# Performance work log

Measured on AMD Instinct MI355X. Metric: run time of the kernel, lower is better.

Reference implementation:

```python
import jax, jax.numpy as jnp
import numpy as np

S, B, D, F, E, K = 1024, 2, 512, 2048, 8, 2


def setup_inputs() -> dict:
    key = jax.random.key(0)
    ks = jax.random.split(key, 12)
    s = lambda *sh: 1.0 / np.sqrt(sh[0])
    inp = {
        "x": jax.random.normal(ks[0], (S, B, D), dtype=jnp.float32),
        # gate: nn.Linear(d_model, n_experts)
        "Wg": jax.random.normal(ks[1], (D, E), dtype=jnp.float32) * s(D),
        "bg": jnp.zeros((E,), dtype=jnp.float32),
        # routed experts: stacked FFN params (E copies of expert)
        "W1": jax.random.normal(ks[2], (E, D, F), dtype=jnp.float32) * s(D),
        "b1": jnp.zeros((E, F), dtype=jnp.float32),
        "W2": jax.random.normal(ks[3], (E, F, D), dtype=jnp.float32) * s(F),
        "b2": jnp.zeros((E, D), dtype=jnp.float32),
        # shared expert (single FFN)
        "Ws1": jax.random.normal(ks[4], (D, F), dtype=jnp.float32) * s(D),
        "bs1": jnp.zeros((F,), dtype=jnp.float32),
        "Ws2": jax.random.normal(ks[5], (F, D), dtype=jnp.float32) * s(F),
        "bs2": jnp.zeros((D,), dtype=jnp.float32),
    }
    return inp


def reference(x, Wg, bg, W1, b1, W2, b2, Ws1, bs1, Ws2, bs2):
    # gate_logits: (S, B, E)
    gate_logits = jnp.einsum("sbd,de->sbe", x, Wg) + bg
    # top-k per token (eval mode: k = n_experts_per_token, t = 1.0)
    weights, selected = jax.lax.top_k(gate_logits, K)  # (S,B,K)
    weights = jax.nn.softmax(weights.astype(jnp.float32), axis=-1)
    # combine weights per expert: (S,B,E)
    onehot = jax.nn.one_hot(selected, E, dtype=weights.dtype)  # (S,B,K,E)
    comb = jnp.einsum("sbk,sbke->sbe", weights, onehot)
    # routed experts computed densely, combined with per-token routing weight
    h = jax.nn.relu(jnp.einsum("sbd,edf->sbef", x, W1) + b1)  # (S,B,E,F)
    y = jnp.einsum("sbef,efd->sbed", h, W2) + b2              # (S,B,E,D)
    out = jnp.einsum("sbe,sbed->sbd", comb, y)
    # shared expert, scaled by 1/k
    hs = jax.nn.relu(jnp.einsum("sbd,df->sbf", x, Ws1) + bs1)
    shared = jnp.einsum("sbf,fd->sbd", hs, Ws2) + bs2
    out = out + (1.0 / K) * shared
    return out
```

## Files before the change

### kernel.cpp

```cpp
#include <hip/hip_runtime.h>
#include <hip/hip_bf16.h>
#include <stdint.h>

#define TT 2048
#define DD 512
#define FF 2048
#define EE 8

typedef unsigned short u16;
typedef __attribute__((ext_vector_type(8))) unsigned short ushort8v;
typedef __attribute__((ext_vector_type(8))) short short8;
typedef __attribute__((ext_vector_type(4))) float float4v;

__device__ __forceinline__ u16 f2bf(float f) {
    unsigned u = __float_as_uint(f);
    u += 0x7FFF + ((u >> 16) & 1);
    return (u16)(u >> 16);
}

__device__ __forceinline__ void gl_lds16(const u16* g, u16* l) {
    __builtin_amdgcn_global_load_lds(
        (const __attribute__((address_space(1))) unsigned int*)g,
        (__attribute__((address_space(3))) unsigned int*)l, 16, 0, 0);
}

#define WS_HB   0ull
#define WS_XG   (WS_HB + 6144ull*2048*2)
#define WS_WT1  (WS_XG + 2048ull*512*2)
#define WS_ME   (WS_WT1 + 9ull*2048*512*2)
#define WS_MW   (WS_ME + 16384)
#define WS_RT   (WS_MW + 16384)
#define WS_WROW (WS_RT + 16384)
#define WS_TROW (WS_WROW + 16384)
#define WS_RTG  (WS_TROW + 16384)
#define WS_WT2  (WS_RTG + 128)
#define WS_NEED (WS_WT2 + 9ull*2048*512*2)

__device__ __forceinline__ void conv_unit(int j, const float* __restrict__ srcE,
                                          const float* __restrict__ srcS,
                                          u16* __restrict__ dst,
                                          int R, int C, int shC, u16* Ls) {
    int mid = j >> 8, t2 = j & 255;
    int tr = t2 >> shC, tc = t2 & ((1 << shC) - 1);
    int r0 = tr * 64, c0 = tc * 64;
    const float* src = (mid < 8) ? srcE + (size_t)mid * R * C : srcS;
    u16* dstm = dst + (size_t)mid * R * C;
    int t = threadIdx.x;
#pragma unroll
    for (int i = 0; i < 4; ++i) {
        int rr = (t >> 4) + i * 16;
        int cc = (t & 15) * 4;
        float4v v = *(const float4v*)(src + (size_t)(r0 + rr) * C + c0 + cc);
#pragma unroll
        for (int jx = 0; jx < 4; ++jx) Ls[(cc + jx) * 72 + rr] = f2bf(v[jx]);
    }
    __syncthreads();
#pragma unroll
    for (int jj = 0; jj < 2; ++jj) {
        int slot = t + jj * 256;
        int cc = slot >> 3, r8 = (slot & 7) * 8;
        ushort8v o = *(const ushort8v*)&Ls[cc * 72 + r8];
        *(ushort8v*)(dstm + (size_t)(c0 + cc) * R + r0 + r8) = o;
    }
}

__device__ __forceinline__ void gate_wave(int t, int lane,
                                          const float* __restrict__ x,
                                          const float* __restrict__ Wg,
                                          const float* __restrict__ bg,
                                          int* __restrict__ metaE,
                                          float* __restrict__ metaW,
                                          u16* __restrict__ xg) {
    const float* xp = x + (size_t)t * DD + lane * 8;
    float4v x0 = *(const float4v*)xp;
    float4v x1 = *(const float4v*)(xp + 4);
    float xf[8] = {x0[0], x0[1], x0[2], x0[3], x1[0], x1[1], x1[2], x1[3]};
    float acc[EE] = {0.f, 0.f, 0.f, 0.f, 0.f, 0.f, 0.f, 0.f};
#pragma unroll
    for (int g = 0; g < 8; ++g) {
        const float* wp = Wg + (size_t)(lane * 8 + g) * EE;
        float4v w0 = *(const float4v*)wp;
        float4v w1 = *(const float4v*)(wp + 4);
        acc[0] += xf[g] * w0[0]; acc[1] += xf[g] * w0[1];
        acc[2] += xf[g] * w0[2]; acc[3] += xf[g] * w0[3];
        acc[4] += xf[g] * w1[0]; acc[5] += xf[g] * w1[1];
        acc[6] += xf[g] * w1[2]; acc[7] += xf[g] * w1[3];
    }
#pragma unroll
    for (int off = 1; off < 64; off <<= 1) {
#pragma unroll
        for (int e = 0; e < EE; ++e) acc[e] += __shfl_xor(acc[e], off, 64);
    }
    ushort8v xv;
#pragma unroll
    for (int jx = 0; jx < 4; ++jx) xv[jx] = f2bf(x0[jx]);
#pragma unroll
    for (int jx = 0; jx < 4; ++jx) xv[4 + jx] = f2bf(x1[jx]);
    *(ushort8v*)(xg + (size_t)t * DD + lane * 8) = xv;
    if (lane == 0) {
#pragma unroll
        for (int e = 0; e < EE; ++e) acc[e] += bg[e];
        int e0 = 0; float l0 = acc[0];
#pragma unroll
        for (int e = 1; e < EE; ++e) if (acc[e] > l0) { l0 = acc[e]; e0 = e; }
        int e1 = -1; float l1 = -3.4e38f;
#pragma unroll
        for (int e = 0; e < EE; ++e)
            if (e != e0 && acc[e] > l1) { l1 = acc[e]; e1 = e; }
        float ex = __expf(l1 - l0);
        float w0 = 1.f / (1.f + ex);
        metaE[2 * t] = e0; metaE[2 * t + 1] = e1;
        metaW[2 * t] = w0; metaW[2 * t + 1] = 1.f - w0;
    }
}

__global__ __launch_bounds__(256) void fused1_k(
    const float* __restrict__ x, const float* __restrict__ Wg,
    const float* __restrict__ bg,
    const float* __restrict__ W1, const float* __restrict__ Ws1,
    const float* __restrict__ W2, const float* __restrict__ Ws2,
    float* __restrict__ out, u16* __restrict__ xg,
    u16* __restrict__ Wt1, u16* __restrict__ Wt2,
    int* __restrict__ metaE, float* __restrict__ metaW, int nconv) {
    __shared__ __align__(16) u16 Ls[64 * 72];
    int b = blockIdx.x, tid = threadIdx.x;
    if (b < nconv) {
        if (b < 2304) conv_unit(b, W1, Ws1, Wt1, DD, FF, 5, Ls);
        else          conv_unit(b - 2304, W2, Ws2, Wt2, FF, DD, 3, Ls);
    } else if (b < nconv + 512) {
        int gb = b - nconv;
        gate_wave(gb * 4 + (tid >> 6), tid & 63, x, Wg, bg, metaE, metaW, xg);
    } else {
        int zb = b - nconv - 512;
        float* op = out + (size_t)zb * 8192;
#pragma unroll
        for (int it = 0; it < 8; ++it)
            *(float4v*)(op + it * 1024 + tid * 4) = (float4v){0.f, 0.f, 0.f, 0.f};
    }
}

__global__ __launch_bounds__(256) void conv2_k(const float* __restrict__ W2,
                                               const float* __restrict__ Ws2,
                                               u16* __restrict__ Wt2) {
    __shared__ __align__(16) u16 Ls[64 * 72];
    conv_unit(blockIdx.x, W2, Ws2, Wt2, FF, DD, 3, Ls);
}

__global__ __launch_bounds__(256) void rank_k(const int* __restrict__ metaE,
                                              const float* __restrict__ metaW,
                                              int* __restrict__ routing,
                                              int* __restrict__ rtok,
                                              float* __restrict__ wrow,
                                              int* __restrict__ trow) {
    __shared__ __align__(16) char smem[16384];
    u16* er      = (u16*)smem;
    int* segCnt  = (int*)(smem + 8192);
    int* segBase = (int*)(smem + 10240);
    int* expTot  = (int*)(smem + 12288);
    int tid = threadIdx.x, wv = tid >> 6, lane = tid & 63;
    unsigned long long below = (lane == 0) ? 0ull : ((~0ull) >> (64 - lane));
    for (int s = wv * 16; s < wv * 16 + 16; ++s) {
        int entry = s * 64 + lane;
        int e = metaE[entry];
        int rk = 0;
#pragma unroll
        for (int ee = 0; ee < 8; ++ee) {
            unsigned long long m = __ballot(e == ee);
            if (e == ee) rk = __popcll(m & below);
            if (lane == ee) segCnt[s * 8 + ee] = __popcll(m);
        }
        er[entry] = (u16)(e | (rk << 4));
    }
    __syncthreads();
    if (tid < 8) {
        int s = 0;
        for (int g = 0; g < 64; ++g) { segBase[g * 8 + tid] = s; s += segCnt[g * 8 + tid]; }
        expTot[tid] = s;
    }
    __syncthreads();
    if (tid == 0) {
        int s = 0;
        for (int e = 0; e < 8; ++e) { int c = expTot[e]; expTot[8 + e] = s; s += c; }
    }
    __syncthreads();
    if (tid < 8) { routing[tid] = expTot[8 + tid]; routing[8 + tid] = expTot[tid]; }
    for (int i = 0; i < 16; ++i) {
        int entry = tid + i * 256;
        int v = er[entry];
        int e = v & 15, rk = v >> 4;
        int row = expTot[8 + e] + segBase[(entry >> 6) * 8 + e] + rk;
        rtok[row] = entry >> 1;
        wrow[row] = metaW[entry];
        trow[entry] = row;
    }
}

__global__ __launch_bounds__(256) void gemmA_k(
    const u16* __restrict__ xg, const u16* __restrict__ Wt1,
    const float* __restrict__ b1, const float* __restrict__ bs1,
    const int* __restrict__ routing, const int* __restrict__ rtok,
    u16* __restrict__ hbuf) {
    __shared__ __align__(16) u16 As[2][64 * 64];
    __shared__ __align__(16) u16 Bs[2][128 * 64];
    const int* offs = routing; const int* cnt = routing + 8;
    int j = blockIdx.x, tid = threadIdx.x;
    int rt, ct, Mloc, hRowBase, rowBase; bool routed;
    const u16* Bsrc; const float* bias;
    if (j < 512) {
        rt = j >> 4; ct = j & 15; Mloc = 64; rowBase = rt * 64;
        Bsrc = Wt1 + (size_t)8 * FF * DD; bias = bs1;
        hRowBase = 4096 + rt * 64; routed = false;
    } else {
        int jr = j - 512; int e = jr & 7; int rc = jr >> 3;
        rt = rc >> 4; ct = rc & 15;
        int M = cnt[e]; if (rt * 64 >= M) return;
        Mloc = M - rt * 64; if (Mloc > 64) Mloc = 64;
        rowBase = offs[e] + rt * 64;
        Bsrc = Wt1 + (size_t)e * FF * DD; bias = b1 + e * FF;
        hRowBase = rowBase; routed = true;
    }
    int n0 = ct * 128;
    int lane = tid & 63, w = tid >> 6, ln = lane & 15, quad = lane >> 4;
    int lr8 = lane >> 3;
    int cs = (lane & 7) ^ lr8;
    const u16* ApS[2];
#pragma unroll
    for (int i = 0; i < 2; ++i) {
        int r = w * 16 + i * 8 + lr8;
        int tok;
        if (routed) { int br = rowBase + r; if (br > 4095) br = 4095; tok = rtok[br]; }
        else tok = rowBase + r;
        ApS[i] = xg + (size_t)tok * DD + cs * 8;
    }
    const u16* BpS[4];
#pragma unroll
    for (int i = 0; i < 4; ++i) {
        int r = w * 32 + i * 8 + lr8;
        BpS[i] = Bsrc + (size_t)(n0 + r) * DD + cs * 8;
    }
    float4v acc[2][4];
#pragma unroll
    for (int a = 0; a < 2; ++a)
#pragma unroll
        for (int b = 0; b < 4; ++b) acc[a][b] = (float4v){0.f, 0.f, 0.f, 0.f};

    auto stage = [&](int kt, int pb) {
        u16* Ab = &As[pb][0]; u16* Bb = &Bs[pb][0];
#pragma unroll
        for (int i = 0; i < 2; ++i)
            gl_lds16(ApS[i] + kt * 64, Ab + (w * 16 + i * 8) * 64);
#pragma unroll
        for (int i = 0; i < 4; ++i)
            gl_lds16(BpS[i] + kt * 64, Bb + (w * 32 + i * 8) * 64);
    };

    stage(0, 0);
#pragma unroll
    for (int kt = 0; kt < 8; ++kt) {
        int pb = kt & 1;
        if (kt < 7) {
            stage(kt + 1, pb ^ 1);
            asm volatile("s_waitcnt vmcnt(6)" ::: "memory");
        } else {
            asm volatile("s_waitcnt vmcnt(0)" ::: "memory");
        }
        __builtin_amdgcn_s_barrier();
        __builtin_amdgcn_sched_barrier(0);
        const u16* Ab = &As[pb][0]; const u16* Bb = &Bs[pb][0];
#pragma unroll
        for (int s = 0; s < 2; ++s) {
            int chs = ((s * 4 + quad) ^ (ln & 7)) * 8;
            short8 Af[2], Bf[4];
#pragma unroll
            for (int a = 0; a < 2; ++a) {
                int ra = (w & 1) * 32 + a * 16 + ln;
                Af[a] = *(const short8*)(Ab + ra * 64 + chs);
            }
#pragma unroll
            for (int b = 0; b < 4; ++b) {
                int rb = (w >> 1) * 64 + b * 16 + ln;
                Bf[b] = *(const short8*)(Bb + rb * 64 + chs);
            }
#pragma unroll
            for (int a = 0; a < 2; ++a)
#pragma unroll
                for (int b = 0; b < 4; ++b)
                    acc[a][b] = __builtin_amdgcn_mfma_f32_16x16x32_bf16(Af[a], Bf[b], acc[a][b], 0, 0, 0);
        }
        __builtin_amdgcn_sched_barrier(0);
        __builtin_amdgcn_s_barrier();
    }
#pragma unroll
    for (int b = 0; b < 4; ++b) {
        int n = n0 + (w >> 1) * 64 + b * 16 + ln;
        float bv = bias[n];
#pragma unroll
        for (int a = 0; a < 2; ++a) {
#pragma unroll
            for (int i = 0; i < 4; ++i) {
                int lr = (w & 1) * 32 + a * 16 + quad * 4 + i;
                if (lr < Mloc) {
                    float v = acc[a][b][i] + bv;
                    v = v > 0.f ? v : 0.f;
                    hbuf[(size_t)(hRowBase + lr) * FF + n] = f2bf(v);
                }
            }
        }
    }
}

__global__ __launch_bounds__(512) void gemmB_k(
    const u16* __restrict__ hbuf, const u16* __restrict__ Wt2,
    const float* __restrict__ b2, const float* __restrict__ bs2,
    const int* __restrict__ routing, float* __restrict__ ybuf) {
    __shared__ __align__(16) u16 As[2][64 * 64];
    __shared__ __align__(16) u16 Bs[2][128 * 64];
    const int* offs = routing; const int* cnt = routing + 8;
    int j = blockIdx.x, tid = threadIdx.x;
    int rt, ct, Mloc, aRowBase;
    const u16* Bsrc; const float* bias;
    if (j < 128) {
        rt = j >> 2; ct = j & 3;
        Mloc = 64; aRowBase = 4096 + rt * 64;
        Bsrc = Wt2 + (size_t)8 * DD * FF; bias = bs2;
    } else {
        int jr = j - 128; int e = jr & 7; int rc = jr >> 3;
        rt = rc >> 2; ct = rc & 3;
        int M = cnt[e]; if (rt * 64 >= M) return;
        Mloc = M - rt * 64; if (Mloc > 64) Mloc = 64;
        aRowBase = offs[e] + rt * 64;
        Bsrc = Wt2 + (size_t)e * DD * FF; bias = b2 + e * DD;
    }
    int n0 = ct * 128;
    int lane = tid & 63, w = tid >> 6, ln = lane & 15, quad = lane >> 4;
    int wm = w >> 2, wn = w & 3;
    int lr8 = lane >> 3;
    int cs = (lane & 7) ^ lr8;
    const u16* ApS = hbuf + (size_t)(aRowBase + w * 8 + lr8) * FF + cs * 8;
    const u16* BpS[2];
#pragma unroll
    for (int i = 0; i < 2; ++i)
        BpS[i] = Bsrc + (size_t)(n0 + w * 16 + i * 8 + lr8) * FF + cs * 8;
    float4v acc[2][2];
#pragma unroll
    for (int a = 0; a < 2; ++a)
#pragma unroll
        for (int b = 0; b < 2; ++b) acc[a][b] = (float4v){0.f, 0.f, 0.f, 0.f};

    auto stage = [&](int kt, int pb) {
        gl_lds16(ApS + kt * 64, &As[pb][0] + (w * 8) * 64);
#pragma unroll
        for (int i = 0; i < 2; ++i)
            gl_lds16(BpS[i] + kt * 64, &Bs[pb][0] + (w * 16 + i * 8) * 64);
    };

    stage(0, 0);
#pragma unroll
    for (int kt = 0; kt < 32; ++kt) {
        int pb = kt & 1;
        if (kt < 31) {
            stage(kt + 1, pb ^ 1);
            asm volatile("s_waitcnt vmcnt(3)" ::: "memory");
        } else {
            asm volatile("s_waitcnt vmcnt(0)" ::: "memory");
        }
        __builtin_amdgcn_s_barrier();
        __builtin_amdgcn_sched_barrier(0);
        const u16* Ab = &As[pb][0]; const u16* Bb = &Bs[pb][0];
#pragma unroll
        for (int s = 0; s < 2; ++s) {
            int chs = ((s * 4 + quad) ^ (ln & 7)) * 8;
            short8 Af[2], Bf[2];
#pragma unroll
            for (int a = 0; a < 2; ++a) {
                int ra = wm * 32 + a * 16 + ln;
                Af[a] = *(const short8*)(Ab + ra * 64 + chs);
            }
#pragma unroll
            for (int b = 0; b < 2; ++b) {
                int rb = wn * 32 + b * 16 + ln;
                Bf[b] = *(const short8*)(Bb + rb * 64 + chs);
            }
#pragma unroll
            for (int a = 0; a < 2; ++a)
#pragma unroll
                for (int b = 0; b < 2; ++b)
                    acc[a][b] = __builtin_amdgcn_mfma_f32_16x16x32_bf16(Af[a], Bf[b], acc[a][b], 0, 0, 0);
        }
        __builtin_amdgcn_sched_barrier(0);
        __builtin_amdgcn_s_barrier();
    }
#pragma unroll
    for (int b = 0; b < 2; ++b) {
        int n = n0 + wn * 32 + b * 16 + ln;
        float bv = bias[n];
#pragma unroll
        for (int a = 0; a < 2; ++a) {
#pragma unroll
            for (int i = 0; i < 4; ++i) {
                int lr = wm * 32 + a * 16 + quad * 4 + i;
                if (lr < Mloc)
                    ybuf[(size_t)(aRowBase + lr) * DD + n] = acc[a][b][i] + bv;
            }
        }
    }
}

__global__ __launch_bounds__(256) void combine_k(
    const float* __restrict__ ybuf, const int* __restrict__ trow,
    const float* __restrict__ metaW, float* __restrict__ out) {
    int tid = threadIdx.x;
    int tok = blockIdx.x * 2 + (tid >> 7);
    int q = (tid & 127) * 4;
    int r0 = trow[2 * tok], r1 = trow[2 * tok + 1];
    float w0 = metaW[2 * tok], w1 = metaW[2 * tok + 1];
    float4v y0 = *(const float4v*)(ybuf + (size_t)r0 * DD + q);
    float4v y1 = *(const float4v*)(ybuf + (size_t)r1 * DD + q);
    float4v ys = *(const float4v*)(ybuf + (size_t)(4096 + tok) * DD + q);
    float4v o;
#pragma unroll
    for (int i = 0; i < 4; ++i) o[i] = w0 * y0[i] + w1 * y1[i] + 0.5f * ys[i];
    *(float4v*)(out + (size_t)tok * DD + q) = o;
}

__global__ __launch_bounds__(256) void gemmBat_k(
    const u16* __restrict__ hbuf, const u16* __restrict__ Wt2,
    const float* __restrict__ b2, const float* __restrict__ bs2,
    const int* __restrict__ routing, const int* __restrict__ rtok,
    const float* __restrict__ wrow, float* __restrict__ out) {
    __shared__ __align__(16) u16 As[2][64 * 64];
    __shared__ __align__(16) u16 Bs[2][128 * 64];
    const int* offs = routing; const int* cnt = routing + 8;
    int j = blockIdx.x, tid = threadIdx.x;
    int rt, ct, ks, Mloc, aRowBase; bool sh;
    const u16* Bsrc; const float* bias;
    if (j < 256) {
        sh = true; rt = j >> 3; int sub = j & 7; ct = sub >> 1; ks = sub & 1;
        Mloc = 64; aRowBase = 4096 + rt * 64;
        Bsrc = Wt2 + (size_t)8 * DD * FF; bias = bs2;
    } else {
        sh = false; int jr = j - 256; int e = jr & 7; int rc = jr >> 3;
        rt = rc >> 3; ct = (rc >> 1) & 3; ks = rc & 1;
        int M = cnt[e]; if (rt * 64 >= M) return;
        Mloc = M - rt * 64; if (Mloc > 64) Mloc = 64;
        aRowBase = offs[e] + rt * 64;
        Bsrc = Wt2 + (size_t)e * DD * FF; bias = b2 + e * DD;
    }
    int n0 = ct * 128;
    int lane = tid & 63, w = tid >> 6, ln = lane & 15, quad = lane >> 4;
    int lr8 = lane >> 3;
    int cs = (lane & 7) ^ lr8;
    const u16* ApS[2];
#pragma unroll
    for (int i = 0; i < 2; ++i) {
        int r = w * 16 + i * 8 + lr8;
        ApS[i] = hbuf + (size_t)(aRowBase + r) * FF + ks * 1024 + cs * 8;
    }
    const u16* BpS[4];
#pragma unroll
    for (int i = 0; i < 4; ++i) {
        int r = w * 32 + i * 8 + lr8;
        BpS[i] = Bsrc + (size_t)(n0 + r) * FF + ks * 1024 + cs * 8;
    }
    float4v acc[2][4];
#pragma unroll
    for (int a = 0; a < 2; ++a)
#pragma unroll
        for (int b = 0; b < 4; ++b) acc[a][b] = (float4v){0.f, 0.f, 0.f, 0.f};
    auto stage = [&](int kt, int pb) {
        u16* Ab = &As[pb][0]; u16* Bb = &Bs[pb][0];
#pragma unroll
        for (int i = 0; i < 2; ++i)
            gl_lds16(ApS[i] + kt * 64, Ab + (w * 16 + i * 8) * 64);
#pragma unroll
        for (int i = 0; i < 4; ++i)
            gl_lds16(BpS[i] + kt * 64, Bb + (w * 32 + i * 8) * 64);
    };
    stage(0, 0);
#pragma unroll
    for (int kt = 0; kt < 16; ++kt) {
        int pb = kt & 1;
        if (kt < 15) {
            stage(kt + 1, pb ^ 1);
            asm volatile("s_waitcnt vmcnt(6)" ::: "memory");
        } else {
            asm volatile("s_waitcnt vmcnt(0)" ::: "memory");
        }
        __builtin_amdgcn_s_barrier();
        __builtin_amdgcn_sched_barrier(0);
        const u16* Ab = &As[pb][0]; const u16* Bb = &Bs[pb][0];
#pragma unroll
        for (int s = 0; s < 2; ++s) {
            int chs = ((s * 4 + quad) ^ (ln & 7)) * 8;
            short8 Af[2], Bf[4];
#pragma unroll
            for (int a = 0; a < 2; ++a) {
                int ra = (w & 1) * 32 + a * 16 + ln;
                Af[a] = *(const short8*)(Ab + ra * 64 + chs);
            }
#pragma unroll
            for (int b = 0; b < 4; ++b) {
                int rb = (w >> 1) * 64 + b * 16 + ln;
                Bf[b] = *(const short8*)(Bb + rb * 64 + chs);
            }
#pragma unroll
            for (int a = 0; a < 2; ++a)
#pragma unroll
                for (int b = 0; b < 4; ++b)
                    acc[a][b] = __builtin_amdgcn_mfma_f32_16x16x32_bf16(Af[a], Bf[b], acc[a][b], 0, 0, 0);
        }
        __builtin_amdgcn_sched_barrier(0);
        __builtin_amdgcn_s_barrier();
    }
    float bv[4];
#pragma unroll
    for (int b = 0; b < 4; ++b)
        bv[b] = (ks == 0) ? bias[n0 + (w >> 1) * 64 + b * 16 + ln] : 0.f;
#pragma unroll
    for (int a = 0; a < 2; ++a) {
#pragma unroll
        for (int i = 0; i < 4; ++i) {
            int lr = (w & 1) * 32 + a * 16 + quad * 4 + i;
            if (lr < Mloc) {
                int row = aRowBase + lr;
                int t; float wr;
                if (sh) { t = row - 4096; wr = 0.5f; }
                else    { t = rtok[row]; wr = wrow[row]; }
                float* op = out + (size_t)t * DD;
#pragma unroll
                for (int b = 0; b < 4; ++b) {
                    int n = n0 + (w >> 1) * 64 + b * 16 + ln;
                    atomicAdd(op + n, wr * (acc[a][b][i] + bv[b]));
                }
            }
        }
    }
}

extern "C" void kernel_launch(void* const* d_in, const int* in_sizes, int n_in,
                              void* d_out, int out_size, void* d_ws, size_t ws_size,
                              hipStream_t stream) {
    const float* x   = (const float*)d_in[0];
    const float* Wg  = (const float*)d_in[1];
    const float* bg  = (const float*)d_in[2];
    const float* W1  = (const float*)d_in[3];
    const float* b1  = (const float*)d_in[4];
    const float* W2  = (const float*)d_in[5];
    const float* b2  = (const float*)d_in[6];
    const float* Ws1 = (const float*)d_in[7];
    const float* bs1 = (const float*)d_in[8];
    const float* Ws2 = (const float*)d_in[9];
    const float* bs2 = (const float*)d_in[10];
    float* out = (float*)d_out;

    char* ws = (char*)d_ws;
    u16*   hbuf    = (u16*)(ws + WS_HB);
    u16*   xg      = (u16*)(ws + WS_XG);
    u16*   Wt1     = (u16*)(ws + WS_WT1);
    int*   metaE   = (int*)(ws + WS_ME);
    float* metaW   = (float*)(ws + WS_MW);
    int*   rtok    = (int*)(ws + WS_RT);
    float* wrow    = (float*)(ws + WS_WROW);
    int*   trow    = (int*)(ws + WS_TROW);
    int*   routing = (int*)(ws + WS_RTG);
    bool   big     = ws_size >= WS_NEED;
    u16*   Wt2     = big ? (u16*)(ws + WS_WT2) : Wt1;
    float* ybuf    = (float*)(ws + WS_WT1);
    int    nconv   = big ? 4608 : 2304;
    int    ngrid1  = big ? (nconv + 512) : (nconv + 640);

    fused1_k<<<ngrid1, 256, 0, stream>>>(x, Wg, bg, W1, Ws1, W2, Ws2,
                                         out, xg, Wt1, Wt2, metaE, metaW, nconv);
    rank_k<<<1, 256, 0, stream>>>(metaE, metaW, routing, rtok, wrow, trow);
    gemmA_k<<<8704, 256, 0, stream>>>(xg, Wt1, b1, bs1, routing, rtok, hbuf);
    if (big) {
        gemmB_k<<<2176, 512, 0, stream>>>(hbuf, Wt2, b2, bs2, routing, ybuf);
        combine_k<<<1024, 256, 0, stream>>>(ybuf, trow, metaW, out);
    } else {
        conv2_k<<<2304, 256, 0, stream>>>(W2, Ws2, Wt2);
        gemmBat_k<<<4352, 256, 0, stream>>>(hbuf, Wt2, b2, bs2, routing, rtok, wrow, out);
    }
}
```

Baseline: 209.1 us.

## Enlarge GEMM tiles to 128 rows with 512 threads and split-K second GEMM

The first expert GEMM now uses 128x128 output tiles with 8 waves per block instead of 64x128 with 4 waves, halving the grid and the number of weight-tile reloads. The second GEMM also moves to 128-row tiles and splits K into two halves that write separate partial-sum buffers, which the combine kernel then adds. This is meant to raise data reuse per block while keeping enough blocks in flight. In exchange it needs a larger workspace for two fp32 partial buffers and extra combine reads, and it wastes more work on partially filled routed tiles.

```diff
diff --git a/kernel.cpp b/kernel.cpp
--- a/kernel.cpp
+++ b/kernel.cpp
@@ -34,7 +34,9 @@
 #define WS_TROW (WS_WROW + 16384)
 #define WS_RTG  (WS_TROW + 16384)
 #define WS_WT2  (WS_RTG + 128)
-#define WS_NEED (WS_WT2 + 9ull*2048*512*2)
+#define WS_YB   (WS_WT2 + 9ull*2048*512*2)
+#define YS      (6144ull*512)
+#define WS_NEED (WS_YB + 2ull*6144*512*4)
 
 __device__ __forceinline__ void conv_unit(int j, const float* __restrict__ srcE,
                                           const float* __restrict__ srcS,
@@ -195,32 +197,33 @@
     }
 }
 
-__global__ __launch_bounds__(256) void gemmA_k(
+__global__ __launch_bounds__(512) void gemmA_k(
     const u16* __restrict__ xg, const u16* __restrict__ Wt1,
     const float* __restrict__ b1, const float* __restrict__ bs1,
     const int* __restrict__ routing, const int* __restrict__ rtok,
     u16* __restrict__ hbuf) {
-    __shared__ __align__(16) u16 As[2][64 * 64];
+    __shared__ __align__(16) u16 As[2][128 * 64];
     __shared__ __align__(16) u16 Bs[2][128 * 64];
     const int* offs = routing; const int* cnt = routing + 8;
     int j = blockIdx.x, tid = threadIdx.x;
     int rt, ct, Mloc, hRowBase, rowBase; bool routed;
     const u16* Bsrc; const float* bias;
-    if (j < 512) {
-        rt = j >> 4; ct = j & 15; Mloc = 64; rowBase = rt * 64;
+    if (j < 256) {
+        rt = j >> 4; ct = j & 15; Mloc = 128; rowBase = rt * 128;
         Bsrc = Wt1 + (size_t)8 * FF * DD; bias = bs1;
-        hRowBase = 4096 + rt * 64; routed = false;
+        hRowBase = 4096 + rt * 128; routed = false;
     } else {
-        int jr = j - 512; int e = jr & 7; int rc = jr >> 3;
+        int jr = j - 256; int e = jr & 7; int rc = jr >> 3;
         rt = rc >> 4; ct = rc & 15;
-        int M = cnt[e]; if (rt * 64 >= M) return;
-        Mloc = M - rt * 64; if (Mloc > 64) Mloc = 64;
-        rowBase = offs[e] + rt * 64;
+        int M = cnt[e]; if (rt * 128 >= M) return;
+        Mloc = M - rt * 128; if (Mloc > 128) Mloc = 128;
+        rowBase = offs[e] + rt * 128;
         Bsrc = Wt1 + (size_t)e * FF * DD; bias = b1 + e * FF;
         hRowBase = rowBase; routed = true;
     }
     int n0 = ct * 128;
     int lane = tid & 63, w = tid >> 6, ln = lane & 15, quad = lane >> 4;
+    int wm = w >> 2, wn = w & 3;
     int lr8 = lane >> 3;
     int cs = (lane & 7) ^ lr8;
     const u16* ApS[2];
@@ -232,26 +235,25 @@
         else tok = rowBase + r;
         ApS[i] = xg + (size_t)tok * DD + cs * 8;
     }
-    const u16* BpS[4];
-#pragma unroll
-    for (int i = 0; i < 4; ++i) {
-        int r = w * 32 + i * 8 + lr8;
+    const u16* BpS[2];
+#pragma unroll
+    for (int i = 0; i < 2; ++i) {
+        int r = w * 16 + i * 8 + lr8;
         BpS[i] = Bsrc + (size_t)(n0 + r) * DD + cs * 8;
     }
-    float4v acc[2][4];
-#pragma unroll
-    for (int a = 0; a < 2; ++a)
-#pragma unroll
-        for (int b = 0; b < 4; ++b) acc[a][b] = (float4v){0.f, 0.f, 0.f, 0.f};
+    float4v acc[4][2];
+#pragma unroll
+    for (int a = 0; a < 4; ++a)
+#pragma unroll
+        for (int b = 0; b < 2; ++b) acc[a][b] = (float4v){0.f, 0.f, 0.f, 0.f};
 
     auto stage = [&](int kt, int pb) {
-        u16* Ab = &As[pb][0]; u16* Bb = &Bs[pb][0];
 #pragma unroll
         for (int i = 0; i < 2; ++i)
-            gl_lds16(ApS[i] + kt * 64, Ab + (w * 16 + i * 8) * 64);
-#pragma unroll
-        for (int i = 0; i < 4; ++i)
-            gl_lds16(BpS[i] + kt * 64, Bb + (w * 32 + i * 8) * 64);
+            gl_lds16(ApS[i] + kt * 64, &As[pb][0] + (w * 16 + i * 8) * 64);
+#pragma unroll
+        for (int i = 0; i < 2; ++i)
+            gl_lds16(BpS[i] + kt * 64, &Bs[pb][0] + (w * 16 + i * 8) * 64);
     };
 
     stage(0, 0);
@@ -260,7 +262,7 @@
         int pb = kt & 1;
         if (kt < 7) {
             stage(kt + 1, pb ^ 1);
-            asm volatile("s_waitcnt vmcnt(6)" ::: "memory");
+            asm volatile("s_waitcnt vmcnt(4)" ::: "memory");
         } else {
             asm volatile("s_waitcnt vmcnt(0)" ::: "memory");
         }
@@ -270,35 +272,35 @@
 #pragma unroll
         for (int s = 0; s < 2; ++s) {
             int chs = ((s * 4 + quad) ^ (ln & 7)) * 8;
-            short8 Af[2], Bf[4];
-#pragma unroll
-            for (int a = 0; a < 2; ++a) {
-                int ra = (w & 1) * 32 + a * 16 + ln;
+            short8 Af[4], Bf[2];
+#pragma unroll
+            for (int a = 0; a < 4; ++a) {
+                int ra = wm * 64 + a * 16 + ln;
                 Af[a] = *(const short8*)(Ab + ra * 64 + chs);
             }
 #pragma unroll
-            for (int b = 0; b < 4; ++b) {
-                int rb = (w >> 1) * 64 + b * 16 + ln;
+            for (int b = 0; b < 2; ++b) {
+                int rb = wn * 32 + b * 16 + ln;
                 Bf[b] = *(const short8*)(Bb + rb * 64 + chs);
             }
 #pragma unroll
-            for (int a = 0; a < 2; ++a)
-#pragma unroll
-                for (int b = 0; b < 4; ++b)
+            for (int a = 0; a < 4; ++a)
+#pragma unroll
+                for (int b = 0; b < 2; ++b)
                     acc[a][b] = __builtin_amdgcn_mfma_f32_16x16x32_bf16(Af[a], Bf[b], acc[a][b], 0, 0, 0);
         }
         __builtin_amdgcn_sched_barrier(0);
         __builtin_amdgcn_s_barrier();
     }
 #pragma unroll
-    for (int b = 0; b < 4; ++b) {
-        int n = n0 + (w >> 1) * 64 + b * 16 + ln;
+    for (int b = 0; b < 2; ++b) {
+        int n = n0 + wn * 32 + b * 16 + ln;
         float bv = bias[n];
 #pragma unroll
-        for (int a = 0; a < 2; ++a) {
+        for (int a = 0; a < 4; ++a) {
 #pragma unroll
             for (int i = 0; i < 4; ++i) {
-                int lr = (w & 1) * 32 + a * 16 + quad * 4 + i;
+                int lr = wm * 64 + a * 16 + quad * 4 + i;
                 if (lr < Mloc) {
                     float v = acc[a][b][i] + bv;
                     v = v > 0.f ? v : 0.f;
@@ -313,22 +315,22 @@
     const u16* __restrict__ hbuf, const u16* __restrict__ Wt2,
     const float* __restrict__ b2, const float* __restrict__ bs2,
     const int* __restrict__ routing, float* __restrict__ ybuf) {
-    __shared__ __align__(16) u16 As[2][64 * 64];
+    __shared__ __align__(16) u16 As[2][128 * 64];
     __shared__ __align__(16) u16 Bs[2][128 * 64];
     const int* offs = routing; const int* cnt = routing + 8;
     int j = blockIdx.x, tid = threadIdx.x;
-    int rt, ct, Mloc, aRowBase;
+    int rt, ct, ks, Mloc, aRowBase;
     const u16* Bsrc; const float* bias;
     if (j < 128) {
-        rt = j >> 2; ct = j & 3;
-        Mloc = 64; aRowBase = 4096 + rt * 64;
+        ks = j & 1; ct = (j >> 1) & 3; rt = j >> 3;
+        Mloc = 128; aRowBase = 4096 + rt * 128;
         Bsrc = Wt2 + (size_t)8 * DD * FF; bias = bs2;
     } else {
         int jr = j - 128; int e = jr & 7; int rc = jr >> 3;
-        rt = rc >> 2; ct = rc & 3;
-        int M = cnt[e]; if (rt * 64 >= M) return;
-        Mloc = M - rt * 64; if (Mloc > 64) Mloc = 64;
-        aRowBase = offs[e] + rt * 64;
+        ks = rc & 1; ct = (rc >> 1) & 3; rt = rc >> 3;
+        int M = cnt[e]; if (rt * 128 >= M) return;
+        Mloc = M - rt * 128; if (Mloc > 128) Mloc = 128;
+        aRowBase = offs[e] + rt * 128;
         Bsrc = Wt2 + (size_t)e * DD * FF; bias = b2 + e * DD;
     }
     int n0 = ct * 128;
@@ -336,19 +338,28 @@
     int wm = w >> 2, wn = w & 3;
     int lr8 = lane >> 3;
     int cs = (lane & 7) ^ lr8;
-    const u16* ApS = hbuf + (size_t)(aRowBase + w * 8 + lr8) * FF + cs * 8;
+    const u16* ApS[2];
+#pragma unroll
+    for (int i = 0; i < 2; ++i) {
+        int r = w * 16 + i * 8 + lr8;
+        ApS[i] = hbuf + (size_t)(aRowBase + r) * FF + ks * 1024 + cs * 8;
+    }
     const u16* BpS[2];
 #pragma unroll
-    for (int i = 0; i < 2; ++i)
-        BpS[i] = Bsrc + (size_t)(n0 + w * 16 + i * 8 + lr8) * FF + cs * 8;
-    float4v acc[2][2];
-#pragma unroll
-    for (int a = 0; a < 2; ++a)
+    for (int i = 0; i < 2; ++i) {
+        int r = w * 16 + i * 8 + lr8;
+        BpS[i] = Bsrc + (size_t)(n0 + r) * FF + ks * 1024 + cs * 8;
+    }
+    float4v acc[4][2];
+#pragma unroll
+    for (int a = 0; a < 4; ++a)
 #pragma unroll
         for (int b = 0; b < 2; ++b) acc[a][b] = (float4v){0.f, 0.f, 0.f, 0.f};
 
     auto stage = [&](int kt, int pb) {
-        gl_lds16(ApS + kt * 64, &As[pb][0] + (w * 8) * 64);
+#pragma unroll
+        for (int i = 0; i < 2; ++i)
+            gl_lds16(ApS[i] + kt * 64, &As[pb][0] + (w * 16 + i * 8) * 64);
 #pragma unroll
         for (int i = 0; i < 2; ++i)
             gl_lds16(BpS[i] + kt * 64, &Bs[pb][0] + (w * 16 + i * 8) * 64);
@@ -356,11 +367,11 @@
 
     stage(0, 0);
 #pragma unroll
-    for (int kt = 0; kt < 32; ++kt) {
+    for (int kt = 0; kt < 16; ++kt) {
         int pb = kt & 1;
-        if (kt < 31) {
+        if (kt < 15) {
             stage(kt + 1, pb ^ 1);
-            asm volatile("s_waitcnt vmcnt(3)" ::: "memory");
+            asm volatile("s_waitcnt vmcnt(4)" ::: "memory");
         } else {
             asm volatile("s_waitcnt vmcnt(0)" ::: "memory");
         }
@@ -370,10 +381,10 @@
 #pragma unroll
         for (int s = 0; s < 2; ++s) {
             int chs = ((s * 4 + quad) ^ (ln & 7)) * 8;
-            short8 Af[2], Bf[2];
-#pragma unroll
-            for (int a = 0; a < 2; ++a) {
-                int ra = wm * 32 + a * 16 + ln;
+            short8 Af[4], Bf[2];
+#pragma unroll
+            for (int a = 0; a < 4; ++a) {
+                int ra = wm * 64 + a * 16 + ln;
                 Af[a] = *(const short8*)(Ab + ra * 64 + chs);
             }
 #pragma unroll
@@ -382,7 +393,7 @@
                 Bf[b] = *(const short8*)(Bb + rb * 64 + chs);
             }
 #pragma unroll
-            for (int a = 0; a < 2; ++a)
+            for (int a = 0; a < 4; ++a)
 #pragma unroll
                 for (int b = 0; b < 2; ++b)
                     acc[a][b] = __builtin_amdgcn_mfma_f32_16x16x32_bf16(Af[a], Bf[b], acc[a][b], 0, 0, 0);
@@ -390,17 +401,18 @@
         __builtin_amdgcn_sched_barrier(0);
         __builtin_amdgcn_s_barrier();
     }
+    float* yb = ybuf + (size_t)ks * YS;
 #pragma unroll
     for (int b = 0; b < 2; ++b) {
         int n = n0 + wn * 32 + b * 16 + ln;
-        float bv = bias[n];
-#pragma unroll
-        for (int a = 0; a < 2; ++a) {
+        float bv = (ks == 0) ? bias[n] : 0.f;
+#pragma unroll
+        for (int a = 0; a < 4; ++a) {
 #pragma unroll
             for (int i = 0; i < 4; ++i) {
-                int lr = wm * 32 + a * 16 + quad * 4 + i;
+                int lr = wm * 64 + a * 16 + quad * 4 + i;
                 if (lr < Mloc)
-                    ybuf[(size_t)(aRowBase + lr) * DD + n] = acc[a][b][i] + bv;
+                    yb[(size_t)(aRowBase + lr) * DD + n] = acc[a][b][i] + bv;
             }
         }
     }
@@ -414,12 +426,18 @@
     int q = (tid & 127) * 4;
     int r0 = trow[2 * tok], r1 = trow[2 * tok + 1];
     float w0 = metaW[2 * tok], w1 = metaW[2 * tok + 1];
-    float4v y0 = *(const float4v*)(ybuf + (size_t)r0 * DD + q);
-    float4v y1 = *(const float4v*)(ybuf + (size_t)r1 * DD + q);
-    float4v ys = *(const float4v*)(ybuf + (size_t)(4096 + tok) * DD + q);
+    const float* ya = ybuf;
+    const float* yb = ybuf + YS;
+    float4v y0a = *(const float4v*)(ya + (size_t)r0 * DD + q);
+    float4v y0b = *(const float4v*)(yb + (size_t)r0 * DD + q);
+    float4v y1a = *(const float4v*)(ya + (size_t)r1 * DD + q);
+    float4v y1b = *(const float4v*)(yb + (size_t)r1 * DD + q);
+    float4v ysa = *(const float4v*)(ya + (size_t)(4096 + tok) * DD + q);
+    float4v ysb = *(const float4v*)(yb + (size_t)(4096 + tok) * DD + q);
     float4v o;
 #pragma unroll
-    for (int i = 0; i < 4; ++i) o[i] = w0 * y0[i] + w1 * y1[i] + 0.5f * ys[i];
+    for (int i = 0; i < 4; ++i)
+        o[i] = w0 * (y0a[i] + y0b[i]) + w1 * (y1a[i] + y1b[i]) + 0.5f * (ysa[i] + ysb[i]);
     *(float4v*)(out + (size_t)tok * DD + q) = o;
 }
 
@@ -565,14 +583,14 @@
     int*   routing = (int*)(ws + WS_RTG);
     bool   big     = ws_size >= WS_NEED;
     u16*   Wt2     = big ? (u16*)(ws + WS_WT2) : Wt1;
-    float* ybuf    = (float*)(ws + WS_WT1);
+    float* ybuf    = (float*)(ws + WS_YB);
     int    nconv   = big ? 4608 : 2304;
     int    ngrid1  = big ? (nconv + 512) : (nconv + 640);
 
     fused1_k<<<ngrid1, 256, 0, stream>>>(x, Wg, bg, W1, Ws1, W2, Ws2,
                                          out, xg, Wt1, Wt2, metaE, metaW, nconv);
     rank_k<<<1, 256, 0, stream>>>(metaE, metaW, routing, rtok, wrow, trow);
-    gemmA_k<<<8704, 256, 0, stream>>>(xg, Wt1, b1, bs1, routing, rtok, hbuf);
+    gemmA_k<<<4352, 512, 0, stream>>>(xg, Wt1, b1, bs1, routing, rtok, hbuf);
     if (big) {
         gemmB_k<<<2176, 512, 0, stream>>>(hbuf, Wt2, b2, bs2, routing, ybuf);
         combine_k<<<1024, 256, 0, stream>>>(ybuf, trow, metaW, out);
```

After: 201.4 us. 1.04x faster.
